# Optimization experiments

Hardware: AMD Instinct MI355X
Metric: run time of the kernel (lower is better)

## Reference

```python
import jax, jax.numpy as jnp
import numpy as np

# DualAttention dims
D_MODEL = 1024
H_SA = 8          # self-attention heads
H_RA = 8          # relational-attention heads
TOTAL_H = H_SA + H_RA
HEAD_DIM = D_MODEL // TOTAL_H   # 64
KEY_DIM = HEAD_DIM              # 64
N_REL = 8
REL_PROJ = HEAD_DIM * H_RA // N_REL  # 64
B, S = 2, 2048


def apply_rope(x, cos, sin):
    # x: [b, s, h, d]; cos/sin: [s, d//2]. Pairs are (0,1),(2,3),... as in
    # llama-style apply_rotary_emb (reshape(..., -1, 2).unbind(-1)).
    xr, xi = x[..., 0::2], x[..., 1::2]
    c = cos[None, :, None, :]
    s_ = sin[None, :, None, :]
    out = jnp.stack([xr * c - xi * s_, xr * s_ + xi * c], axis=-1)
    return out.reshape(x.shape)


def setup_inputs() -> dict:
    key = jax.random.key(0)
    ks = jax.random.split(key, 16)
    def w(k, shape):
        return jax.random.normal(k, shape, jnp.float32) * 0.02
    x = jax.random.normal(ks[0], (B, S, D_MODEL), jnp.float32)
    symbols = jax.random.normal(ks[1], (B, S, D_MODEL), jnp.float32)
    # real RoPE tables
    pos = np.arange(S, dtype=np.float32)[:, None]
    inv = 1.0 / (10000.0 ** (np.arange(0, KEY_DIM, 2, dtype=np.float32) / KEY_DIM))
    ang = pos * inv[None, :]
    freqs_cos = jnp.asarray(np.cos(ang), jnp.float32)
    freqs_sin = jnp.asarray(np.sin(ang), jnp.float32)
    return dict(
        x=x, symbols=symbols, freqs_cos=freqs_cos, freqs_sin=freqs_sin,
        # self-attention branch (torch Linear weights: [out, in])
        wq_sa=w(ks[2], (H_SA * KEY_DIM, D_MODEL)),
        wk_sa=w(ks[3], (H_SA * KEY_DIM, D_MODEL)),
        wv_sa=w(ks[4], (H_SA * HEAD_DIM, D_MODEL)),
        wo_sa=w(ks[5], (H_SA * HEAD_DIM, H_SA * HEAD_DIM)),
        # relational-attention branch
        wq_attn=w(ks[6], (H_RA * KEY_DIM, D_MODEL)),
        wk_attn=w(ks[7], (H_RA * KEY_DIM, D_MODEL)),
        wq_rel=w(ks[8], (N_REL * REL_PROJ, D_MODEL)),
        wk_rel=w(ks[9], (N_REL * REL_PROJ, D_MODEL)),
        wr=w(ks[10], (H_RA, HEAD_DIM, N_REL)),
        wv_ra=w(ks[11], (H_RA * HEAD_DIM, D_MODEL)),
        wo_ra=w(ks[12], (H_RA * HEAD_DIM, H_RA * HEAD_DIM)),
    )


def reference(x, symbols, freqs_cos, freqs_sin,
              wq_sa, wk_sa, wv_sa, wo_sa,
              wq_attn, wk_attn, wq_rel, wk_rel, wr, wv_ra, wo_ra):
    b, s, _ = x.shape
    attn_scale = 1.0 / np.sqrt(HEAD_DIM).astype(np.float32)
    rel_scale = 1.0 / np.sqrt(REL_PROJ).astype(np.float32)
    causal = jnp.tril(jnp.ones((s, s), dtype=bool))
    neg = jnp.finfo(x.dtype).min

    def heads(t, h, d):
        return t.reshape(b, s, h, d)

    # ---- self-attention branch (causal SDPA with RoPE) ----
    q = apply_rope(heads(x @ wq_sa.T, H_SA, KEY_DIM), freqs_cos, freqs_sin)
    k = apply_rope(heads(x @ wk_sa.T, H_SA, KEY_DIM), freqs_cos, freqs_sin)
    v = heads(x @ wv_sa.T, H_SA, HEAD_DIM)
    scores = jnp.einsum('bihd,bjhd->bhij', q, k) * attn_scale
    a = jax.nn.softmax(jnp.where(causal, scores, neg), axis=-1)
    sa_out = jnp.einsum('bhij,bjhd->bihd', a, v).reshape(b, s, H_SA * HEAD_DIM) @ wo_sa.T

    # ---- relational-attention branch ----
    # attention scores (softmax selection), with RoPE
    qa = apply_rope(heads(x @ wq_attn.T, H_RA, KEY_DIM), freqs_cos, freqs_sin)
    ka = apply_rope(heads(x @ wk_attn.T, H_RA, KEY_DIM), freqs_cos, freqs_sin)
    ra_scores = jnp.einsum('bihd,bjhd->bhij', qa, ka) * attn_scale
    alpha = jax.nn.softmax(jnp.where(causal, ra_scores, neg), axis=-1)
    # relations r(x_i, x_j) in R^{N_REL} (identity rel_activation)
    qr = heads(x @ wq_rel.T, N_REL, REL_PROJ)
    kr = heads(x @ wk_rel.T, N_REL, REL_PROJ)
    rel = jnp.einsum('birp,bjrp->brij', qr, kr) * rel_scale  # [b, R, i, j]
    # symbol values: wv applied to retrieved symbols
    sv = heads(symbols @ wv_ra.T, H_RA, HEAD_DIM)
    attended_sym = jnp.einsum('bhij,bjhd->bihd', alpha, sv)          # [b, i, h, d]
    attended_rel = jnp.einsum('bhij,brij->bihr', alpha, rel)         # [b, i, h, R]
    rel_out = jnp.einsum('bihr,hdr->bihd', attended_rel, wr)
    ra_out = (attended_sym + rel_out).reshape(b, s, H_RA * HEAD_DIM) @ wo_ra.T

    # DualAttention: concat branch outputs along feature dim -> [b, s, d_model]
    return jnp.concatenate([sa_out, ra_out], axis=-1)
```

## Files before the change

### kernel.cpp

```cpp
#include <hip/hip_runtime.h>

#define B_   2
#define S_   2048
#define H_   8
#define D_   64
#define DM_  1024
#define PJ_  512
#define NT_  32
#define NTRI 528
#define NCHK 80

typedef short bf16x8 __attribute__((ext_vector_type(8)));
typedef float f32x4 __attribute__((ext_vector_type(4)));

__device__ __forceinline__ float bf2f(unsigned int u) {
  return __uint_as_float(u << 16);
}
__device__ __forceinline__ unsigned short f2bf(float f) {
  unsigned int u = __float_as_uint(f);
  u += 0x7fffu + ((u >> 16) & 1u);
  return (unsigned short)(u >> 16);
}

__device__ __forceinline__ void glds16(const unsigned short* g, unsigned short* l) {
  __builtin_amdgcn_global_load_lds(
      (const __attribute__((address_space(1))) void*)g,
      (__attribute__((address_space(3))) void*)l, 16, 0, 0);
}

struct CvtJobs {
  const float*    src[12];
  unsigned short* dst[12];
  int             n4[12];
};

__global__ __launch_bounds__(256) void cvt_many(CvtJobs J) {
  const int j = blockIdx.y;
  const int i = blockIdx.x * 256 + threadIdx.x;
  if (i >= J.n4[j]) return;
  const float4 v = ((const float4*)J.src[j])[i];
  ushort4 o;
  o.x = f2bf(v.x); o.y = f2bf(v.y); o.z = f2bf(v.z); o.w = f2bf(v.w);
  ((ushort4*)J.dst[j])[i] = o;
}

__device__ __forceinline__
void gemm128_glds(const unsigned short* __restrict__ A, int m0,
                  const unsigned short* __restrict__ Wb,
                  unsigned short* __restrict__ Cb, int ldc, int KD,
                  unsigned short* As, unsigned short* Bs)
{
  const int tid = threadIdx.x;
  const int wv = tid >> 6, lane = tid & 63;
  const int r15 = lane & 15, quad = lane >> 4;
  const int wm = (wv >> 1) * 64, wn = (wv & 1) * 64;
  f32x4 acc[4][4];
#pragma unroll
  for (int i = 0; i < 4; ++i)
#pragma unroll
    for (int j = 0; j < 4; ++j) acc[i][j] = (f32x4){0.f, 0.f, 0.f, 0.f};

  const int srow = wv * 16 + (lane >> 2);
  const int scol = ((lane & 3) ^ ((lane >> 3) & 3)) * 8;
  const unsigned short* gaA0 = A + (size_t)(m0 + srow) * KD + scol;
  const unsigned short* gaA1 = gaA0 + (size_t)64 * KD;
  const unsigned short* gaB0 = Wb + (size_t)srow * KD + scol;
  const unsigned short* gaB1 = gaB0 + (size_t)64 * KD;
  unsigned short* ldsA0 = As + wv * 512;
  unsigned short* ldsA1 = As + 2048 + wv * 512;
  unsigned short* ldsB0 = Bs + wv * 512;
  unsigned short* ldsB1 = Bs + 2048 + wv * 512;
  const int rxor = (r15 >> 1) & 3;

  for (int kk = 0; kk < KD; kk += 32) {
    __syncthreads();
    glds16(gaA0 + kk, ldsA0);
    glds16(gaA1 + kk, ldsA1);
    glds16(gaB0 + kk, ldsB0);
    glds16(gaB1 + kk, ldsB1);
    __syncthreads();
    bf16x8 af[4], bf[4];
#pragma unroll
    for (int i = 0; i < 4; ++i)
      af[i] = *(const bf16x8*)(As + (wm + i * 16 + r15) * 32 + ((quad ^ rxor) << 3));
#pragma unroll
    for (int j = 0; j < 4; ++j)
      bf[j] = *(const bf16x8*)(Bs + (wn + j * 16 + r15) * 32 + ((quad ^ rxor) << 3));
#pragma unroll
    for (int i = 0; i < 4; ++i)
#pragma unroll
      for (int j = 0; j < 4; ++j)
        acc[i][j] = __builtin_amdgcn_mfma_f32_16x16x32_bf16(af[i], bf[j], acc[i][j], 0, 0, 0);
  }
#pragma unroll
  for (int i = 0; i < 4; ++i)
#pragma unroll
    for (int r = 0; r < 4; ++r) {
      unsigned short* cp = Cb + (size_t)(wm + i * 16 + quad * 4 + r) * ldc + wn + r15;
#pragma unroll
      for (int j = 0; j < 4; ++j) cp[j * 16] = f2bf(acc[i][j][r]);
    }
}

__global__ __launch_bounds__(256)
void proj_tiled(const unsigned short* __restrict__ XB,
                const unsigned short* __restrict__ SYB,
                const unsigned short* __restrict__ Wcat,
                unsigned short* __restrict__ Qbase,
                unsigned short* __restrict__ SV)
{
  __shared__ unsigned short As[128 * 32];
  __shared__ unsigned short Bs[128 * 32];
  const int m0 = blockIdx.x * 128;
  const int ny = blockIdx.y;
  const size_t NB = (size_t)B_ * S_ * PJ_;
  const unsigned short* A;
  const unsigned short* Wb;
  unsigned short* Cb;
  if (ny < 28) {
    const int n0 = ny * 128;
    A  = XB;
    Wb = Wcat + (size_t)n0 * DM_;
    Cb = Qbase + (size_t)(n0 >> 9) * NB + (size_t)m0 * PJ_ + (n0 & 511);
  } else {
    const int n0 = (ny - 28) * 128;
    A  = SYB;
    Wb = Wcat + (size_t)7 * PJ_ * DM_ + (size_t)n0 * DM_;
    Cb = SV + (size_t)m0 * PJ_ + n0;
  }
  gemm128_glds(A, m0, Wb, Cb, PJ_, DM_, As, Bs);
}

__global__ __launch_bounds__(256)
void out_tiled(const unsigned short* __restrict__ Asa,
               const unsigned short* __restrict__ Ara,
               const unsigned short* __restrict__ WOSA,
               const unsigned short* __restrict__ WORA,
               float* __restrict__ Out)
{
  __shared__ unsigned short As[128 * 40];
  __shared__ unsigned short Bs[64 * 40];
  const int m0 = blockIdx.x * 128;
  const int ny = blockIdx.y;
  const int n0 = (ny & 7) * 64;
  const unsigned short* A  = (ny < 8) ? Asa : Ara;
  const unsigned short* Wb = ((ny < 8) ? WOSA : WORA) + (size_t)n0 * PJ_;
  float* Cb = Out + (size_t)m0 * DM_ + ((ny < 8) ? 0 : 512) + n0;

  const int tid = threadIdx.x;
  const int wv = tid >> 6, lane = tid & 63;
  const int r15 = lane & 15, quad = lane >> 4;
  const int wm = wv * 32;
  f32x4 acc[2][4];
#pragma unroll
  for (int i = 0; i < 2; ++i)
#pragma unroll
    for (int j = 0; j < 4; ++j) acc[i][j] = (f32x4){0.f, 0.f, 0.f, 0.f};

  const int arow = tid >> 1, ac = (tid & 1) * 16;
  const int brow = tid >> 2, bc = (tid & 3) * 8;
  const unsigned short* ga = A + (size_t)(m0 + arow) * PJ_ + ac;
  const unsigned short* gb = Wb + (size_t)brow * PJ_ + bc;
  unsigned short* la = As + arow * 40 + ac;
  unsigned short* lb = Bs + brow * 40 + bc;

  for (int kk = 0; kk < PJ_; kk += 32) {
    __syncthreads();
    const uint4 a0 = *(const uint4*)(ga + kk);
    const uint4 a1 = *(const uint4*)(ga + kk + 8);
    const uint4 b0 = *(const uint4*)(gb + kk);
    *(uint4*)la       = a0;
    *(uint4*)(la + 8) = a1;
    *(uint4*)lb       = b0;
    __syncthreads();
    bf16x8 af[2], bf[4];
#pragma unroll
    for (int i = 0; i < 2; ++i)
      af[i] = *(const bf16x8*)(As + (wm + i * 16 + r15) * 40 + quad * 8);
#pragma unroll
    for (int j = 0; j < 4; ++j)
      bf[j] = *(const bf16x8*)(Bs + (j * 16 + r15) * 40 + quad * 8);
#pragma unroll
    for (int i = 0; i < 2; ++i)
#pragma unroll
      for (int j = 0; j < 4; ++j)
        acc[i][j] = __builtin_amdgcn_mfma_f32_16x16x32_bf16(af[i], bf[j], acc[i][j], 0, 0, 0);
  }
#pragma unroll
  for (int i = 0; i < 2; ++i)
#pragma unroll
    for (int r = 0; r < 4; ++r) {
      float* cp = Cb + (size_t)(wm + i * 16 + quad * 4 + r) * DM_ + r15;
#pragma unroll
      for (int j = 0; j < 4; ++j) cp[j * 16] = acc[i][j][r];
    }
}

__global__ __launch_bounds__(256)
void rel_gemm(const unsigned short* __restrict__ QRg, const unsigned short* __restrict__ KRg,
              unsigned short* __restrict__ RelCF)
{
  __shared__ unsigned short As[128 * 72];
  __shared__ unsigned short Bs[128 * 72];
  const int t = blockIdx.x;
  int I = 0;
  while ((I + 1) * (I + 2) / 2 <= t) ++I;
  const int J = t - I * (I + 1) / 2;
  const int rr = blockIdx.y & 7, b = blockIdx.y >> 3;
  const int tid = threadIdx.x;
  const int wv = tid >> 6, lane = tid & 63;
  const int r15 = lane & 15, quad = lane >> 4;

  const int srow = tid >> 1, c32 = (tid & 1) * 32;
  const unsigned short* ga = QRg + (size_t)(b * S_ + I * 128 + srow) * PJ_ + rr * 64 + c32;
  const unsigned short* gb = KRg + (size_t)(b * S_ + J * 128 + srow) * PJ_ + rr * 64 + c32;
  unsigned short* la = As + srow * 72 + c32;
  unsigned short* lb = Bs + srow * 72 + c32;
#pragma unroll
  for (int q = 0; q < 4; ++q) {
    *(uint4*)(la + q * 8) = *(const uint4*)(ga + q * 8);
    *(uint4*)(lb + q * 8) = *(const uint4*)(gb + q * 8);
  }
  __syncthreads();

  const int wm = (wv >> 1) * 64, wn = (wv & 1) * 64;
  const int it64 = 2 * I + (wv >> 1), jt64 = 2 * J + (wv & 1);
  if (jt64 > it64) return;
  f32x4 acc[4][4];
#pragma unroll
  for (int i = 0; i < 4; ++i)
#pragma unroll
    for (int j = 0; j < 4; ++j) acc[i][j] = (f32x4){0.f, 0.f, 0.f, 0.f};
#pragma unroll
  for (int k0 = 0; k0 < 2; ++k0) {
    bf16x8 af[4], bf[4];
#pragma unroll
    for (int i = 0; i < 4; ++i)
      af[i] = *(const bf16x8*)(As + (wm + i * 16 + r15) * 72 + quad * 8 + k0 * 32);
#pragma unroll
    for (int j = 0; j < 4; ++j)
      bf[j] = *(const bf16x8*)(Bs + (wn + j * 16 + r15) * 72 + quad * 8 + k0 * 32);
#pragma unroll
    for (int i = 0; i < 4; ++i)
#pragma unroll
      for (int j = 0; j < 4; ++j)
        acc[i][j] = __builtin_amdgcn_mfma_f32_16x16x32_bf16(af[i], bf[j], acc[i][j], 0, 0, 0);
  }
  unsigned short* out = RelCF + ((size_t)(b * 8 + rr) * NTRI + (size_t)it64 * (it64 + 1) / 2 + jt64) * 4096;
#pragma unroll
  for (int i = 0; i < 4; ++i) {
    unsigned short tmp[16];
#pragma unroll
    for (int j = 0; j < 4; ++j)
#pragma unroll
      for (int r = 0; r < 4; ++r)
        tmp[j * 4 + r] = f2bf(acc[i][j][r] * 0.125f);
    unsigned short* op = out + (size_t)(i * 64 + lane) * 16;
    *(uint4*)op       = *(const uint4*)tmp;
    *(uint4*)(op + 8) = *(const uint4*)(tmp + 8);
  }
}

__global__ __launch_bounds__(256)
void rope_kernel(unsigned short* Q, unsigned short* K,
                 unsigned short* QA, unsigned short* KA,
                 const float* __restrict__ fc,
                 const float* __restrict__ fs) {
  const int idx = blockIdx.x * 256 + threadIdx.x;
  const int t  = idx >> 20;
  const int r  = idx & 0xFFFFF;
  const int ci = r & 31;
  const int h  = (r >> 5) & 7;
  const int s  = (r >> 8) & 2047;
  const int b  = r >> 19;
  unsigned short* P = (t == 0) ? Q : (t == 1) ? K : (t == 2) ? QA : KA;
  const size_t off = ((size_t)(b * S_ + s)) * PJ_ + h * D_ + (ci << 1);
  const float xr = bf2f(P[off]);
  const float xi = bf2f(P[off + 1]);
  const float cs = fc[s * 32 + ci];
  const float sn = fs[s * 32 + ci];
  P[off]     = f2bf(xr * cs - xi * sn);
  P[off + 1] = f2bf(xr * sn + xi * cs);
}

__global__ __launch_bounds__(256)
void flash_part(const unsigned short* __restrict__ Qsa, const unsigned short* __restrict__ Ksa,
                const unsigned short* __restrict__ Vsa,
                const unsigned short* __restrict__ Qra, const unsigned short* __restrict__ Kra,
                const unsigned short* __restrict__ SVra,
                const unsigned short* __restrict__ RelCF,
                unsigned short* __restrict__ PoP, float* __restrict__ lP,
                float* __restrict__ arpP)
{
  __shared__ unsigned short Ks[2][64][72];
  __shared__ unsigned short Vt[2][64][72];
  __shared__ unsigned short Ps[64][72];
  const int x = blockIdx.x;
  int it, c;
  if (x < 8)       { it = x;                    c = 0; }
  else if (x < 24) { it = 8 + ((x - 8) >> 1);   c = (x - 8) & 1; }
  else if (x < 48) { it = 16 + (x - 24) / 3;    c = (x - 24) % 3; }
  else             { it = 24 + ((x - 48) >> 2); c = (x - 48) & 3; }
  const int j0 = c * 8;
  const int jend = (j0 + 8 < it + 1) ? (j0 + 8) : (it + 1);
  const bool ra = (blockIdx.y >= 8);
  const int h = blockIdx.y & 7;
  const int b = blockIdx.z;
  const int chunkId = (b * 16 + (int)blockIdx.y) * NCHK + x;
  const unsigned short* Qg = ra ? Qra : Qsa;
  const unsigned short* Kg = ra ? Kra : Ksa;
  const unsigned short* Vg = ra ? SVra : Vsa;
  const int tid = threadIdx.x;
  const int wv = tid >> 6, lane = tid & 63;
  const int r15 = lane & 15, quad = lane >> 4;
  const size_t bh = (size_t)b * S_ * PJ_ + (size_t)h * D_;
  const size_t relStride = (size_t)NTRI * 4096;

  const int kr0 = tid >> 3, kc0 = (tid & 7) << 3;
  const int kr1 = (tid + 256) >> 3;
  const unsigned short* kgp = Kg + bh + kc0;
  const unsigned short* vgp = Vg + bh + (size_t)lane * PJ_ + wv * 8;

  const unsigned short* qp = Qg + bh + (size_t)(it * 64 + wv * 16 + r15) * PJ_ + quad * 8;
  const bf16x8 aq0 = *(const bf16x8*)qp;
  const bf16x8 aq1 = *(const bf16x8*)(qp + 32);

  unsigned short one8[8];
#pragma unroll
  for (int i = 0; i < 8; ++i) one8[i] = 0x3F80;
  const bf16x8 ones = *(const bf16x8*)one8;

  f32x4 o_acc[4];
  f32x4 l_acc = {0.f, 0.f, 0.f, 0.f};
  float arp[4][8];
#pragma unroll
  for (int n = 0; n < 4; ++n) o_acc[n] = (f32x4){0.f, 0.f, 0.f, 0.f};
#pragma unroll
  for (int r = 0; r < 4; ++r)
#pragma unroll
    for (int rr = 0; rr < 8; ++rr) arp[r][rr] = 0.f;
  const int row0 = it * 64 + wv * 16 + quad * 4;
  const size_t relTileBase = (size_t)(b * 8) * NTRI * 4096
                           + (size_t)(it * (it + 1)) / 2 * 4096
                           + (size_t)(wv * 64 + lane) * 16;

  uint4 ka0, ka1, va0, va1;
  {
    const size_t jb = (size_t)j0 * 64 * PJ_;
    ka0 = *(const uint4*)(kgp + jb + (size_t)kr0 * PJ_);
    ka1 = *(const uint4*)(kgp + jb + (size_t)kr1 * PJ_);
    va0 = *(const uint4*)(vgp + jb);
    va1 = *(const uint4*)(vgp + jb + 32);
  }
  int p = 0;
  {
    *(uint4*)&Ks[0][kr0][kc0] = ka0;
    *(uint4*)&Ks[0][kr1][kc0] = ka1;
    unsigned short t8[8];
    *(uint4*)t8 = va0;
#pragma unroll
    for (int m = 0; m < 8; ++m) Vt[0][wv * 8 + m][lane] = t8[m];
    *(uint4*)t8 = va1;
#pragma unroll
    for (int m = 0; m < 8; ++m) Vt[0][wv * 8 + 32 + m][lane] = t8[m];
  }
  __syncthreads();

  for (int jt = j0; jt < jend; ++jt) {
    const bool more = (jt + 1 < jend);
    if (more) {
      const size_t jb = (size_t)(jt + 1) * 64 * PJ_;
      ka0 = *(const uint4*)(kgp + jb + (size_t)kr0 * PJ_);
      ka1 = *(const uint4*)(kgp + jb + (size_t)kr1 * PJ_);
      va0 = *(const uint4*)(vgp + jb);
      va1 = *(const uint4*)(vgp + jb + 32);
    }
    uint4 pre[8];
    const unsigned short* rtBase = RelCF + relTileBase + (size_t)jt * 4096;
    if (ra) {
      const unsigned short* rt = rtBase;
#pragma unroll
      for (int q = 0; q < 4; ++q) {
        pre[2 * q]     = *(const uint4*)rt;
        pre[2 * q + 1] = *(const uint4*)(rt + 8);
        rt += relStride;
      }
    }
    f32x4 s[4];
#pragma unroll
    for (int n = 0; n < 4; ++n) s[n] = (f32x4){0.f, 0.f, 0.f, 0.f};
#pragma unroll
    for (int k0 = 0; k0 < 2; ++k0) {
      const bf16x8 af = k0 ? aq1 : aq0;
#pragma unroll
      for (int n = 0; n < 4; ++n) {
        const bf16x8 bf = *(const bf16x8*)&Ks[p][n * 16 + r15][quad * 8 + k0 * 32];
        s[n] = __builtin_amdgcn_mfma_f32_16x16x32_bf16(af, bf, s[n], 0, 0, 0);
      }
    }
    if (jt == it) {
#pragma unroll
      for (int n = 0; n < 4; ++n)
#pragma unroll
        for (int r = 0; r < 4; ++r) {
          const bool ok = (jt * 64 + n * 16 + r15 <= row0 + r);
          s[n][r] = ok ? __expf(s[n][r] * 0.125f - 4.0f) : 0.f;
        }
    } else {
#pragma unroll
      for (int n = 0; n < 4; ++n)
#pragma unroll
        for (int r = 0; r < 4; ++r)
          s[n][r] = __expf(s[n][r] * 0.125f - 4.0f);
    }
#pragma unroll
    for (int n = 0; n < 4; ++n)
#pragma unroll
      for (int r = 0; r < 4; ++r)
        Ps[wv * 16 + quad * 4 + r][n * 16 + r15] = f2bf(s[n][r]);
    if (ra) {
      const unsigned short* rt2 = rtBase + 4 * relStride;
#pragma unroll
      for (int rr = 0; rr < 8; ++rr) {
        unsigned short rv[16];
        if (rr < 4) {
          *(uint4*)rv       = pre[2 * rr];
          *(uint4*)(rv + 8) = pre[2 * rr + 1];
        } else {
          *(uint4*)rv       = *(const uint4*)rt2;
          *(uint4*)(rv + 8) = *(const uint4*)(rt2 + 8);
          rt2 += relStride;
        }
#pragma unroll
        for (int n = 0; n < 4; ++n)
#pragma unroll
          for (int r = 0; r < 4; ++r)
            arp[r][rr] += s[n][r] * bf2f(rv[n * 4 + r]);
      }
    }
#pragma unroll
    for (int k0 = 0; k0 < 2; ++k0) {
      const bf16x8 pf = *(const bf16x8*)&Ps[wv * 16 + r15][quad * 8 + k0 * 32];
#pragma unroll
      for (int n = 0; n < 4; ++n) {
        const bf16x8 vf = *(const bf16x8*)&Vt[p][n * 16 + r15][quad * 8 + k0 * 32];
        o_acc[n] = __builtin_amdgcn_mfma_f32_16x16x32_bf16(pf, vf, o_acc[n], 0, 0, 0);
      }
      l_acc = __builtin_amdgcn_mfma_f32_16x16x32_bf16(pf, ones, l_acc, 0, 0, 0);
    }
    if (more) {
      const int q = p ^ 1;
      *(uint4*)&Ks[q][kr0][kc0] = ka0;
      *(uint4*)&Ks[q][kr1][kc0] = ka1;
      unsigned short t8[8];
      *(uint4*)t8 = va0;
#pragma unroll
      for (int m = 0; m < 8; ++m) Vt[q][wv * 8 + m][lane] = t8[m];
      *(uint4*)t8 = va1;
#pragma unroll
      for (int m = 0; m < 8; ++m) Vt[q][wv * 8 + 32 + m][lane] = t8[m];
      __syncthreads();
      p = q;
    }
  }
  unsigned short* po = PoP + (size_t)chunkId * 4096;
#pragma unroll
  for (int n = 0; n < 4; ++n)
#pragma unroll
    for (int r = 0; r < 4; ++r)
      po[(wv * 16 + quad * 4 + r) * 64 + n * 16 + r15] = f2bf(o_acc[n][r]);
  if (r15 == 0) {
#pragma unroll
    for (int r = 0; r < 4; ++r)
      lP[(size_t)chunkId * 64 + wv * 16 + quad * 4 + r] = l_acc[r];
  }
  if (ra) {
#pragma unroll
    for (int r = 0; r < 4; ++r)
#pragma unroll
      for (int rr = 0; rr < 8; ++rr)
#pragma unroll
        for (int o = 1; o < 16; o <<= 1)
          arp[r][rr] += __shfl_xor(arp[r][rr], o);
    if (r15 == 0) {
#pragma unroll
      for (int r = 0; r < 4; ++r) {
        float* ap = arpP + (size_t)chunkId * 512 + (wv * 16 + quad * 4 + r) * 8;
#pragma unroll
        for (int rr = 0; rr < 8; ++rr) ap[rr] = arp[r][rr];
      }
    }
  }
}

__global__ __launch_bounds__(256)
void flash_merge(const unsigned short* __restrict__ PoP, const float* __restrict__ lP,
                 const float* __restrict__ arpP, const float* __restrict__ wrF,
                 unsigned short* __restrict__ Osa, unsigned short* __restrict__ Ora)
{
  const int it = blockIdx.x;
  const int hh = blockIdx.y;
  const int b  = blockIdx.z;
  const bool ra = (hh >= 8);
  const int h = hh & 7;
  const int nc = it / 8 + 1;
  int cb;
  if (it < 8)       cb = it;
  else if (it < 16) cb = 8 + 2 * (it - 8);
  else if (it < 24) cb = 24 + 3 * (it - 16);
  else              cb = 48 + 4 * (it - 24);
  const int cid0 = (b * 16 + hh) * NCHK + cb;
  const int tid = threadIdx.x;
  const int row = tid >> 2;
  const int cg  = tid & 3;

  float L = 0.f;
  for (int c = 0; c < nc; ++c) L += lP[(size_t)(cid0 + c) * 64 + row];
  const float inv = 1.f / L;

  float o[16];
#pragma unroll
  for (int k = 0; k < 16; ++k) o[k] = 0.f;
  for (int c = 0; c < nc; ++c) {
    const unsigned short* pp = PoP + (size_t)(cid0 + c) * 4096 + row * 64 + cg * 16;
    unsigned short t[16];
    *(uint4*)t       = *(const uint4*)pp;
    *(uint4*)(t + 8) = *(const uint4*)(pp + 8);
#pragma unroll
    for (int k = 0; k < 16; ++k) o[k] += bf2f(t[k]);
  }
  if (ra) {
    float A[8];
#pragma unroll
    for (int rr = 0; rr < 8; ++rr) A[rr] = 0.f;
    for (int c = 0; c < nc; ++c) {
      const float* ap = arpP + (size_t)(cid0 + c) * 512 + row * 8;
#pragma unroll
      for (int rr = 0; rr < 8; ++rr) A[rr] += ap[rr];
    }
#pragma unroll
    for (int k = 0; k < 16; ++k) {
      const float* wp = wrF + ((size_t)h * 64 + cg * 16 + k) * 8;
      float ro = 0.f;
#pragma unroll
      for (int rr = 0; rr < 8; ++rr) ro += A[rr] * wp[rr];
      o[k] += ro;
    }
  }
  const size_t bh = (size_t)b * S_ * PJ_ + (size_t)h * D_;
  unsigned short* op = (ra ? Ora : Osa) + bh + (size_t)(it * 64 + row) * PJ_ + cg * 16;
#pragma unroll
  for (int k = 0; k < 16; ++k) op[k] = f2bf(o[k] * inv);
}

extern "C" void kernel_launch(void* const* d_in, const int* in_sizes, int n_in,
                              void* d_out, int out_size, void* d_ws, size_t ws_size,
                              hipStream_t stream)
{
  (void)in_sizes; (void)n_in; (void)out_size; (void)ws_size;
  const float* x    = (const float*)d_in[0];
  const float* sym  = (const float*)d_in[1];
  const float* fc   = (const float*)d_in[2];
  const float* fs   = (const float*)d_in[3];
  const float* wqsa = (const float*)d_in[4];
  const float* wksa = (const float*)d_in[5];
  const float* wvsa = (const float*)d_in[6];
  const float* wosa = (const float*)d_in[7];
  const float* wqat = (const float*)d_in[8];
  const float* wkat = (const float*)d_in[9];
  const float* wqre = (const float*)d_in[10];
  const float* wkre = (const float*)d_in[11];
  const float* wr   = (const float*)d_in[12];
  const float* wvra = (const float*)d_in[13];
  const float* wora = (const float*)d_in[14];

  unsigned short* wsb = (unsigned short*)d_ws;
  const size_t NX = (size_t)B_ * S_ * DM_;
  const size_t NB = (size_t)B_ * S_ * PJ_;
  const size_t NW = (size_t)PJ_ * DM_;
  const size_t NO = (size_t)PJ_ * PJ_;
  const size_t NR = (size_t)B_ * 8 * NTRI * 4096;
  const size_t NCH = (size_t)B_ * 16 * NCHK;

  size_t off = 0;
  unsigned short* XB   = wsb + off; off += NX;
  unsigned short* SYB  = wsb + off; off += NX;
  unsigned short* WB[8];
  for (int i = 0; i < 8; ++i) { WB[i] = wsb + off; off += NW; }
  unsigned short* WOSA = wsb + off; off += NO;
  unsigned short* WORA = wsb + off; off += NO;
  unsigned short* Q    = wsb + off; off += NB;
  unsigned short* K    = wsb + off; off += NB;
  unsigned short* V    = wsb + off; off += NB;
  unsigned short* QA   = wsb + off; off += NB;
  unsigned short* KA   = wsb + off; off += NB;
  unsigned short* QR   = wsb + off; off += NB;
  unsigned short* KR   = wsb + off; off += NB;
  unsigned short* SV   = wsb + off; off += NB;
  unsigned short* Asa  = wsb + off; off += NB;
  unsigned short* Ara  = wsb + off; off += NB;
  unsigned short* RelCF = wsb + off; off += NR;
  unsigned short* PoP  = XB;
  float* lP   = (float*)(wsb + off); off += NCH * 64 * 2;
  float* arpP = (float*)(wsb + off); off += NCH * 512 * 2;

  CvtJobs cj;
  cj.src[0]  = x;    cj.dst[0]  = XB;    cj.n4[0]  = (int)(NX / 4);
  cj.src[1]  = sym;  cj.dst[1]  = SYB;   cj.n4[1]  = (int)(NX / 4);
  cj.src[2]  = wqsa; cj.dst[2]  = WB[0]; cj.n4[2]  = (int)(NW / 4);
  cj.src[3]  = wksa; cj.dst[3]  = WB[1]; cj.n4[3]  = (int)(NW / 4);
  cj.src[4]  = wvsa; cj.dst[4]  = WB[2]; cj.n4[4]  = (int)(NW / 4);
  cj.src[5]  = wqat; cj.dst[5]  = WB[3]; cj.n4[5]  = (int)(NW / 4);
  cj.src[6]  = wkat; cj.dst[6]  = WB[4]; cj.n4[6]  = (int)(NW / 4);
  cj.src[7]  = wqre; cj.dst[7]  = WB[5]; cj.n4[7]  = (int)(NW / 4);
  cj.src[8]  = wkre; cj.dst[8]  = WB[6]; cj.n4[8]  = (int)(NW / 4);
  cj.src[9]  = wvra; cj.dst[9]  = WB[7]; cj.n4[9]  = (int)(NW / 4);
  cj.src[10] = wosa; cj.dst[10] = WOSA;  cj.n4[10] = (int)(NO / 4);
  cj.src[11] = wora; cj.dst[11] = WORA;  cj.n4[11] = (int)(NO / 4);
  cvt_many<<<dim3(4096, 12), dim3(256), 0, stream>>>(cj);

  proj_tiled<<<dim3(32, 32), dim3(256), 0, stream>>>(XB, SYB, WB[0], Q, SV);
  rope_kernel<<<dim3(16384), dim3(256), 0, stream>>>(Q, K, QA, KA, fc, fs);
  rel_gemm<<<dim3(136, 16), dim3(256), 0, stream>>>(QR, KR, RelCF);
  flash_part<<<dim3(NCHK, 16, B_), dim3(256), 0, stream>>>(
      Q, K, V, QA, KA, SV, RelCF, PoP, lP, arpP);
  flash_merge<<<dim3(NT_, 16, B_), dim3(256), 0, stream>>>(
      PoP, lP, arpP, wr, Asa, Ara);
  out_tiled<<<dim3(32, 16), dim3(256), 0, stream>>>(Asa, Ara, WOSA, WORA, (float*)d_out);
}
```

Measured before the change: 329.6 us.

## Fuse RoPE into relation GEMM kernel with vectorized bf16 unpacking

Removes the separate RoPE launch and folds it into the relation GEMM kernel: after the GEMM tile, each thread applies RoPE to 8 packed bf16 values at a time through 16-byte loads and stores, instead of scalar per-pair accesses. The early return for upper-triangle warps becomes a branch so those warps still do their RoPE share. The flash_part and flash_merge kernels also unpack packed bf16 pairs with a shift and a mask instead of per-element conversion. This saves one launch and issues wider memory accesses, at the cost of more work and register pressure in the GEMM kernel.

After: 325.0 us. Within noise of the previous version (-1.4%).

```diff
diff --git a/kernel.cpp b/kernel.cpp
--- a/kernel.cpp
+++ b/kernel.cpp
@@ -197,8 +197,11 @@
 }
 
 __global__ __launch_bounds__(256)
-void rel_gemm(const unsigned short* __restrict__ QRg, const unsigned short* __restrict__ KRg,
-              unsigned short* __restrict__ RelCF)
+void rel_rope(const unsigned short* __restrict__ QRg, const unsigned short* __restrict__ KRg,
+              unsigned short* __restrict__ RelCF,
+              unsigned short* __restrict__ Qp, unsigned short* __restrict__ Kp,
+              unsigned short* __restrict__ QAp, unsigned short* __restrict__ KAp,
+              const float* __restrict__ fcp, const float* __restrict__ fsp)
 {
   __shared__ unsigned short As[128 * 72];
   __shared__ unsigned short Bs[128 * 72];
@@ -225,62 +228,72 @@
 
   const int wm = (wv >> 1) * 64, wn = (wv & 1) * 64;
   const int it64 = 2 * I + (wv >> 1), jt64 = 2 * J + (wv & 1);
-  if (jt64 > it64) return;
-  f32x4 acc[4][4];
-#pragma unroll
-  for (int i = 0; i < 4; ++i)
-#pragma unroll
-    for (int j = 0; j < 4; ++j) acc[i][j] = (f32x4){0.f, 0.f, 0.f, 0.f};
-#pragma unroll
-  for (int k0 = 0; k0 < 2; ++k0) {
-    bf16x8 af[4], bf[4];
+  if (jt64 <= it64) {
+    f32x4 acc[4][4];
 #pragma unroll
     for (int i = 0; i < 4; ++i)
-      af[i] = *(const bf16x8*)(As + (wm + i * 16 + r15) * 72 + quad * 8 + k0 * 32);
-#pragma unroll
-    for (int j = 0; j < 4; ++j)
-      bf[j] = *(const bf16x8*)(Bs + (wn + j * 16 + r15) * 72 + quad * 8 + k0 * 32);
-#pragma unroll
-    for (int i = 0; i < 4; ++i)
+#pragma unroll
+      for (int j = 0; j < 4; ++j) acc[i][j] = (f32x4){0.f, 0.f, 0.f, 0.f};
+#pragma unroll
+    for (int k0 = 0; k0 < 2; ++k0) {
+      bf16x8 af[4], bf[4];
+#pragma unroll
+      for (int i = 0; i < 4; ++i)
+        af[i] = *(const bf16x8*)(As + (wm + i * 16 + r15) * 72 + quad * 8 + k0 * 32);
 #pragma unroll
       for (int j = 0; j < 4; ++j)
-        acc[i][j] = __builtin_amdgcn_mfma_f32_16x16x32_bf16(af[i], bf[j], acc[i][j], 0, 0, 0);
-  }
-  unsigned short* out = RelCF + ((size_t)(b * 8 + rr) * NTRI + (size_t)it64 * (it64 + 1) / 2 + jt64) * 4096;
-#pragma unroll
-  for (int i = 0; i < 4; ++i) {
-    unsigned short tmp[16];
-#pragma unroll
-    for (int j = 0; j < 4; ++j)
-#pragma unroll
-      for (int r = 0; r < 4; ++r)
-        tmp[j * 4 + r] = f2bf(acc[i][j][r] * 0.125f);
-    unsigned short* op = out + (size_t)(i * 64 + lane) * 16;
-    *(uint4*)op       = *(const uint4*)tmp;
-    *(uint4*)(op + 8) = *(const uint4*)(tmp + 8);
-  }
-}
-
-__global__ __launch_bounds__(256)
-void rope_kernel(unsigned short* Q, unsigned short* K,
-                 unsigned short* QA, unsigned short* KA,
-                 const float* __restrict__ fc,
-                 const float* __restrict__ fs) {
-  const int idx = blockIdx.x * 256 + threadIdx.x;
-  const int t  = idx >> 20;
-  const int r  = idx & 0xFFFFF;
-  const int ci = r & 31;
-  const int h  = (r >> 5) & 7;
-  const int s  = (r >> 8) & 2047;
-  const int b  = r >> 19;
-  unsigned short* P = (t == 0) ? Q : (t == 1) ? K : (t == 2) ? QA : KA;
-  const size_t off = ((size_t)(b * S_ + s)) * PJ_ + h * D_ + (ci << 1);
-  const float xr = bf2f(P[off]);
-  const float xi = bf2f(P[off + 1]);
-  const float cs = fc[s * 32 + ci];
-  const float sn = fs[s * 32 + ci];
-  P[off]     = f2bf(xr * cs - xi * sn);
-  P[off + 1] = f2bf(xr * sn + xi * cs);
+        bf[j] = *(const bf16x8*)(Bs + (wn + j * 16 + r15) * 72 + quad * 8 + k0 * 32);
+#pragma unroll
+      for (int i = 0; i < 4; ++i)
+#pragma unroll
+        for (int j = 0; j < 4; ++j)
+          acc[i][j] = __builtin_amdgcn_mfma_f32_16x16x32_bf16(af[i], bf[j], acc[i][j], 0, 0, 0);
+    }
+    unsigned short* out = RelCF + ((size_t)(b * 8 + rr) * NTRI + (size_t)it64 * (it64 + 1) / 2 + jt64) * 4096;
+#pragma unroll
+    for (int i = 0; i < 4; ++i) {
+      unsigned short tmp[16];
+#pragma unroll
+      for (int j = 0; j < 4; ++j)
+#pragma unroll
+        for (int r = 0; r < 4; ++r)
+          tmp[j * 4 + r] = f2bf(acc[i][j][r] * 0.125f);
+      unsigned short* op = out + (size_t)(i * 64 + lane) * 16;
+      *(uint4*)op       = *(const uint4*)tmp;
+      *(uint4*)(op + 8) = *(const uint4*)(tmp + 8);
+    }
+  }
+
+  const int bid = (int)blockIdx.y * 136 + (int)blockIdx.x;
+  const int gt = bid * 256 + tid;
+#pragma unroll
+  for (int k = 0; k < 2; ++k) {
+    const int i = gt * 2 + k;
+    if (i >= 4 * 262144) continue;
+    const int tn = i >> 18;
+    const int r2 = i & 262143;
+    unsigned short* P = (tn == 0) ? Qp : (tn == 1) ? Kp : (tn == 2) ? QAp : KAp;
+    const int b2 = r2 >> 17;
+    const int s2 = (r2 >> 6) & 2047;
+    const int c8 = (r2 & 63) * 8;
+    const int ci0 = (c8 & 63) >> 1;
+    const size_t off2 = ((size_t)(b2 * S_ + s2)) * PJ_ + c8;
+    uint4 v = *(const uint4*)(P + off2);
+    unsigned int u[4] = {v.x, v.y, v.z, v.w};
+    unsigned int o[4];
+#pragma unroll
+    for (int q = 0; q < 4; ++q) {
+      const float xr = __uint_as_float(u[q] << 16);
+      const float xi = __uint_as_float(u[q] & 0xffff0000u);
+      const float cs = fcp[s2 * 32 + ci0 + q];
+      const float sn = fsp[s2 * 32 + ci0 + q];
+      const unsigned short lo = f2bf(xr * cs - xi * sn);
+      const unsigned short hi = f2bf(xr * sn + xi * cs);
+      o[q] = (unsigned int)lo | ((unsigned int)hi << 16);
+    }
+    uint4 ov; ov.x = o[0]; ov.y = o[1]; ov.z = o[2]; ov.w = o[3];
+    *(uint4*)(P + off2) = ov;
+  }
 }
 
 __global__ __launch_bounds__(256)
@@ -422,20 +435,23 @@
       const unsigned short* rt2 = rtBase + 4 * relStride;
 #pragma unroll
       for (int rr = 0; rr < 8; ++rr) {
-        unsigned short rv[16];
+        unsigned int ru[8];
         if (rr < 4) {
-          *(uint4*)rv       = pre[2 * rr];
-          *(uint4*)(rv + 8) = pre[2 * rr + 1];
+          *(uint4*)ru       = pre[2 * rr];
+          *(uint4*)(ru + 4) = pre[2 * rr + 1];
         } else {
-          *(uint4*)rv       = *(const uint4*)rt2;
-          *(uint4*)(rv + 8) = *(const uint4*)(rt2 + 8);
+          *(uint4*)ru       = *(const uint4*)rt2;
+          *(uint4*)(ru + 4) = *(const uint4*)(rt2 + 8);
           rt2 += relStride;
         }
 #pragma unroll
-        for (int n = 0; n < 4; ++n)
-#pragma unroll
-          for (int r = 0; r < 4; ++r)
-            arp[r][rr] += s[n][r] * bf2f(rv[n * 4 + r]);
+        for (int n = 0; n < 4; ++n) {
+          const unsigned int u0 = ru[2 * n], u1 = ru[2 * n + 1];
+          arp[0][rr] += s[n][0] * __uint_as_float(u0 << 16);
+          arp[1][rr] += s[n][1] * __uint_as_float(u0 & 0xffff0000u);
+          arp[2][rr] += s[n][2] * __uint_as_float(u1 << 16);
+          arp[3][rr] += s[n][3] * __uint_as_float(u1 & 0xffff0000u);
+        }
       }
     }
 #pragma unroll
@@ -523,11 +539,14 @@
   for (int k = 0; k < 16; ++k) o[k] = 0.f;
   for (int c = 0; c < nc; ++c) {
     const unsigned short* pp = PoP + (size_t)(cid0 + c) * 4096 + row * 64 + cg * 16;
-    unsigned short t[16];
-    *(uint4*)t       = *(const uint4*)pp;
-    *(uint4*)(t + 8) = *(const uint4*)(pp + 8);
-#pragma unroll
-    for (int k = 0; k < 16; ++k) o[k] += bf2f(t[k]);
+    unsigned int u[8];
+    *(uint4*)u       = *(const uint4*)pp;
+    *(uint4*)(u + 4) = *(const uint4*)(pp + 8);
+#pragma unroll
+    for (int q = 0; q < 8; ++q) {
+      o[2 * q]     += __uint_as_float(u[q] << 16);
+      o[2 * q + 1] += __uint_as_float(u[q] & 0xffff0000u);
+    }
   }
   if (ra) {
     float A[8];
@@ -620,8 +639,7 @@
   cvt_many<<<dim3(4096, 12), dim3(256), 0, stream>>>(cj);
 
   proj_tiled<<<dim3(32, 32), dim3(256), 0, stream>>>(XB, SYB, WB[0], Q, SV);
-  rope_kernel<<<dim3(16384), dim3(256), 0, stream>>>(Q, K, QA, KA, fc, fs);
-  rel_gemm<<<dim3(136, 16), dim3(256), 0, stream>>>(QR, KR, RelCF);
+  rel_rope<<<dim3(136, 16), dim3(256), 0, stream>>>(QR, KR, RelCF, Q, K, QA, KA, fc, fs);
   flash_part<<<dim3(NCHK, 16, B_), dim3(256), 0, stream>>>(
       Q, K, V, QA, KA, SV, RelCF, PoP, lP, arpP);
   flash_merge<<<dim3(NT_, 16, B_), dim3(256), 0, stream>>>(
```
